# Performance work log

Measured on AMD Instinct MI355X. Metric: run time of the kernel, lower is better.

The kernel has to match this reference:

```python
import jax, jax.numpy as jnp
import numpy as np

C = 256
CK = C // 8  # query/key projection dim

def conv1x1(x, w, b):
    # x: (B,C,H,W), w: (O,C), b: (O,)
    return jnp.einsum('bchw,oc->bohw', x, w) + b[None, :, None, None]

def conv3x3(x, w, b):
    # w: (O,C,3,3)
    y = jax.lax.conv_general_dilated(x, w, window_strides=(1, 1), padding='SAME',
                                     dimension_numbers=('NCHW', 'OIHW', 'NCHW'))
    return y + b[None, :, None, None]

def setup_inputs() -> dict:
    key = jax.random.key(0)
    ks = jax.random.split(key, 24)
    s = 0.05
    d = {
        'x1': jax.random.normal(ks[0], (4, C, 64, 64), jnp.float32),
        'x2': jax.random.normal(ks[1], (4, C, 64, 64), jnp.float32),
        'wq1': jax.random.normal(ks[2], (CK, C), jnp.float32) * s,
        'bq1': jax.random.normal(ks[3], (CK,), jnp.float32) * s,
        'wk1': jax.random.normal(ks[4], (CK, C), jnp.float32) * s,
        'bk1': jax.random.normal(ks[5], (CK,), jnp.float32) * s,
        'wv1': jax.random.normal(ks[6], (C, C), jnp.float32) * s,
        'bv1': jax.random.normal(ks[7], (C,), jnp.float32) * s,
        'wq2': jax.random.normal(ks[8], (CK, C), jnp.float32) * s,
        'bq2': jax.random.normal(ks[9], (CK,), jnp.float32) * s,
        'wk2': jax.random.normal(ks[10], (CK, C), jnp.float32) * s,
        'bk2': jax.random.normal(ks[11], (CK,), jnp.float32) * s,
        'wv2': jax.random.normal(ks[12], (C, C), jnp.float32) * s,
        'bv2': jax.random.normal(ks[13], (C,), jnp.float32) * s,
        'wd1': jax.random.normal(ks[14], (C, C), jnp.float32) * s,
        'bd1': jax.random.normal(ks[15], (C,), jnp.float32) * s,
        'wd3': jax.random.normal(ks[16], (C, C, 3, 3), jnp.float32) * s,
        'bd3': jax.random.normal(ks[17], (C,), jnp.float32) * s,
        'gamma1': jax.random.normal(ks[18], (1,), jnp.float32) * 0.5,
        'gamma2': jax.random.normal(ks[19], (1,), jnp.float32) * 0.5,
    }
    return d

def reference(x1, x2, wq1, bq1, wk1, bk1, wv1, bv1, wq2, bq2, wk2, bk2, wv2, bv2,
              wd1, bd1, wd3, bd3, gamma1, gamma2):
    B, Cc, H, W = x1.shape
    N = H * W
    # projections (1x1 convs), flattened to (B, d, N)
    q1 = conv1x1(x1, wq1, bq1).reshape(B, CK, N)
    k1 = conv1x1(x1, wk1, bk1).reshape(B, CK, N)
    v1 = conv1x1(x1, wv1, bv1).reshape(B, Cc, N)
    q2 = conv1x1(x2, wq2, bq2).reshape(B, CK, N)
    k2 = conv1x1(x2, wk2, bk2).reshape(B, CK, N)
    v2 = conv1x1(x2, wv2, bv2).reshape(B, Cc, N)
    # cross attention 1: queries from x1, keys/values from x2
    energy1 = jnp.einsum('bdi,bdj->bij', q1, k2)          # (B,N,N)
    attn1 = jax.nn.softmax(energy1, axis=-1)
    out1 = jnp.einsum('bcj,bij->bci', v2, attn1).reshape(B, Cc, H, W)
    # cross attention 2: queries from x2, keys/values from x1
    energy2 = jnp.einsum('bdi,bdj->bij', q2, k1)
    attn2 = jax.nn.softmax(energy2, axis=-1)
    out2 = jnp.einsum('bcj,bij->bci', v1, attn2).reshape(B, Cc, H, W)
    # residual conv branches + gamma-scaled skip (norm1/norm2 in source are dead code)
    out1 = out1 + conv1x1(x1, wd1, bd1) + conv3x3(x1, wd3, bd3)
    out2 = out2 + conv1x1(x2, wd1, bd1) + conv3x3(x2, wd3, bd3)
    out1 = x1 + gamma1[0] * out1
    out2 = x2 + gamma2[0] * out2
    return (out1, out2)
```

## Files before the change

### kernel.cpp

```cpp
#include <hip/hip_runtime.h>
#include <hip/hip_bf16.h>

#define CC 256
#define CKD 32
#define NN 4096
#define HH 64
#define WW 64
#define BB 4

#define LOG2E 1.44269504088896f
#define EXPSHIFT 23.0831203874f

typedef __attribute__((ext_vector_type(8))) short short8;
typedef __attribute__((ext_vector_type(4))) float floatx4;

__device__ __forceinline__ unsigned f2bf(float f) {
  union { float f; unsigned u; } v; v.f = f;
  unsigned r = v.u + 0x7fffu + ((v.u >> 16) & 1u);
  return r >> 16;
}
__device__ __forceinline__ float fast_exp2(float x) {
#if __has_builtin(__builtin_amdgcn_exp2f)
  return __builtin_amdgcn_exp2f(x);
#else
  return __expf(x * 0.693147181f);
#endif
}
__device__ __forceinline__ float bf_lo(unsigned u) { return __uint_as_float(u << 16); }
__device__ __forceinline__ float bf_hi(unsigned u) { return __uint_as_float(u & 0xffff0000u); }

__device__ __forceinline__ void bar_lds() {
  asm volatile("s_waitcnt lgkmcnt(0)" ::: "memory");
  __builtin_amdgcn_s_barrier();
}

__global__ __launch_bounds__(256) void pack_kernel(
    const float* __restrict__ x1, const float* __restrict__ x2,
    unsigned short* __restrict__ Xp,
    const float* __restrict__ wd1, const float* __restrict__ wd3,
    const float* __restrict__ wq1, const float* __restrict__ wk1,
    const float* __restrict__ wv1,
    const float* __restrict__ wq2, const float* __restrict__ wk2,
    const float* __restrict__ wv2,
    const float* __restrict__ bq1, const float* __restrict__ bk1,
    const float* __restrict__ bv1,
    const float* __restrict__ bq2, const float* __restrict__ bk2,
    const float* __restrict__ bv2,
    unsigned short* __restrict__ Wp, unsigned short* __restrict__ Wqkv,
    float* __restrict__ Bias) {
  const int t = threadIdx.x;
  __shared__ float tile[64][65];
  if (blockIdx.z < 8) {
    const int nb = blockIdx.x, cbk = blockIdx.y, img = blockIdx.z;
    const float* X = ((img >> 2) ? x2 : x1) + (size_t)(img & 3) * CC * NN;
    const int n0 = nb * 64, c0 = cbk * 64;
    const int nl = t & 63, cl0 = t >> 6;
#pragma unroll
    for (int i = 0; i < 16; ++i)
      tile[cl0 + i * 4][nl] = X[(size_t)(c0 + cl0 + i * 4) * NN + n0 + nl];
    __syncthreads();
#pragma unroll
    for (int it = 0; it < 2; ++it) {
      int id = it * 256 + t;
      int nl2 = id >> 3, cc = id & 7;
      short8 v;
#pragma unroll
      for (int j = 0; j < 8; ++j) v[j] = (short)f2bf(tile[cc * 8 + j][nl2]);
      *(short8*)(Xp + (size_t)img * NN * CC + (size_t)(n0 + nl2) * CC + c0 + cc * 8) = v;
    }
  } else {
    const int id = (blockIdx.y * 64 + blockIdx.x) * 256 + t;
#pragma unroll
    for (int tap = 0; tap < 10; ++tap) {
      float v = (tap < 9) ? wd3[(size_t)id * 9 + tap] : wd1[id];
      Wp[(size_t)tap * (CC * CC) + id] = (unsigned short)f2bf(v);
    }
#pragma unroll
    for (int j = 0; j < 3; ++j) {
      int e = id + j * 65536;
      if (e < 2 * 320 * 256) {
        int inp = e / (320 * 256), rem = e % (320 * 256);
        int o = rem >> 8, c = rem & 255;
        float v;
        if (inp == 0)
          v = (o < 32) ? wq1[o * 256 + c] * LOG2E
              : (o < 64) ? wk1[(o - 32) * 256 + c] : wv1[(o - 64) * 256 + c];
        else
          v = (o < 32) ? wq2[o * 256 + c] * LOG2E
              : (o < 64) ? wk2[(o - 32) * 256 + c] : wv2[(o - 64) * 256 + c];
        Wqkv[e] = (unsigned short)f2bf(v);
      }
    }
    if (id < 640) {
      int inp = id / 320, o = id % 320;
      float v;
      if (inp == 0) v = (o < 32) ? bq1[o] * LOG2E
                        : (o < 64) ? bk1[o - 32] : bv1[o - 64];
      else          v = (o < 32) ? bq2[o] * LOG2E
                        : (o < 64) ? bk2[o - 32] : bv2[o - 64];
      Bias[id] = v;
    }
  }
}

__global__ __launch_bounds__(256) void proj_mfma_kernel(
    const unsigned short* __restrict__ Xp, const unsigned short* __restrict__ Wqkv,
    const float* __restrict__ Bias,
    unsigned short* __restrict__ Qp1, unsigned short* __restrict__ Kp1,
    unsigned short* __restrict__ Vp1,
    unsigned short* __restrict__ Qp2, unsigned short* __restrict__ Kp2,
    unsigned short* __restrict__ Vp2) {
  const int t = threadIdx.x;
  const int w = t >> 6, lane = t & 63;
  const int l15 = lane & 15, g = lane >> 4;
  const int img = blockIdx.x, pb = blockIdx.y;
  const int pix0 = pb * 64;
  const int inp = img >> 2, b = img & 3;
  const unsigned short* Xi = Xp + (size_t)img * NN * CC;
  const unsigned short* Wb = Wqkv + (size_t)inp * 320 * CC;
  const float* Bi = Bias + inp * 320;
  unsigned short* Qp = (inp ? Qp2 : Qp1) + (size_t)b * NN * CKD;
  unsigned short* Kp = (inp ? Kp2 : Kp1) + (size_t)b * NN * CKD;
  unsigned short* Vp = (inp ? Vp2 : Vp1) + (size_t)b * NN * CC;

  __shared__ unsigned short tile[320][72];

  floatx4 acc[4][5];
#pragma unroll
  for (int mf = 0; mf < 4; ++mf)
#pragma unroll
    for (int nf = 0; nf < 5; ++nf) acc[mf][nf] = (floatx4){0.f, 0.f, 0.f, 0.f};
  const int o0w = w * 80;

#pragma unroll
  for (int cb = 0; cb < 8; ++cb) {
    short8 a[4], bfr[5];
#pragma unroll
    for (int mf = 0; mf < 4; ++mf)
      a[mf] = *(const short8*)(Xi + (size_t)(pix0 + mf * 16 + l15) * CC + cb * 32 + g * 8);
#pragma unroll
    for (int nf = 0; nf < 5; ++nf)
      bfr[nf] = *(const short8*)(Wb + (size_t)(o0w + nf * 16 + l15) * CC + cb * 32 + g * 8);
#pragma unroll
    for (int nf = 0; nf < 5; ++nf)
#pragma unroll
      for (int mf = 0; mf < 4; ++mf)
        acc[mf][nf] = __builtin_amdgcn_mfma_f32_16x16x32_bf16(
            a[mf], bfr[nf], acc[mf][nf], 0, 0, 0);
  }

#pragma unroll
  for (int nf = 0; nf < 5; ++nf) {
    float bs = Bi[o0w + nf * 16 + l15];
#pragma unroll
    for (int mf = 0; mf < 4; ++mf) {
      uint2 pk;
      pk.x = f2bf(acc[mf][nf][0] + bs) | (f2bf(acc[mf][nf][1] + bs) << 16);
      pk.y = f2bf(acc[mf][nf][2] + bs) | (f2bf(acc[mf][nf][3] + bs) << 16);
      *(uint2*)&tile[o0w + nf * 16 + l15][mf * 16 + g * 4] = pk;
    }
  }
  __syncthreads();

  {
    const int pix = t >> 2, ch = t & 3;
    short8 vq, vk;
#pragma unroll
    for (int e = 0; e < 8; ++e) {
      vq[e] = (short)tile[ch * 8 + e][pix];
      vk[e] = (short)tile[32 + ch * 8 + e][pix];
    }
    *(short8*)(Qp + (size_t)(pix0 + pix) * CKD + ch * 8) = vq;
    *(short8*)(Kp + (size_t)(pix0 + pix) * CKD + ch * 8) = vk;
  }
#pragma unroll
  for (int it = 0; it < 8; ++it) {
    short8 vv = *(const short8*)&tile[64 + t][it * 8];
    *(short8*)(Vp + ((size_t)((pix0 >> 3) + it) * CC + t) * 8) = vv;
  }
}

__global__ __launch_bounds__(256, 2) void attn_kernel(
    const unsigned short* __restrict__ Qp1, const unsigned short* __restrict__ Kp1,
    const unsigned short* __restrict__ Qp2, const unsigned short* __restrict__ Kp2,
    const unsigned short* __restrict__ Vp1, const unsigned short* __restrict__ Vp2,
    const unsigned short* __restrict__ Xp, const unsigned short* __restrict__ Wp,
    const float* __restrict__ bd1, const float* __restrict__ bd3,
    const float* __restrict__ x1, const float* __restrict__ x2,
    const float* __restrict__ g1, const float* __restrict__ g2,
    float* __restrict__ out) {
  const int t = threadIdx.x;
  const int w = t >> 6, lane = t & 63;
  const int l15 = lane & 15, g = lane >> 4;
  const int att = blockIdx.x, b = blockIdx.y;
  const int yblk = blockIdx.z;
  const int i0 = yblk * 64;

  const unsigned short *Qp, *Kp, *Vp; const float *x; float gamma; float* o;
  if (att == 0) { Qp = Qp1; Kp = Kp2; Vp = Vp2; x = x1; gamma = g1[0]; o = out; }
  else          { Qp = Qp2; Kp = Kp1; Vp = Vp1; x = x2; gamma = g2[0];
                  o = out + (size_t)BB * CC * NN; }
  Qp += (size_t)b * NN * CKD; Kp += (size_t)b * NN * CKD; Vp += (size_t)b * NN * CC;
  x += (size_t)b * CC * NN; o += (size_t)b * CC * NN;
  const unsigned short* Xi = Xp + (size_t)(att * 4 + b) * NN * CC;

  __shared__ union {
    unsigned short ps[4][64][72];
    unsigned short xs[3][66][72];
  } u;
  __shared__ float l_s[64];

  short8 bq = *(const short8*)(Qp + (size_t)(i0 + w * 16 + l15) * CKD + g * 8);

  floatx4 acc[4][4];
#pragma unroll
  for (int a = 0; a < 4; ++a)
#pragma unroll
    for (int c = 0; c < 4; ++c) acc[a][c] = (floatx4){0.f, 0.f, 0.f, 0.f};
  float l_acc = 0.f;
  const floatx4 zinit = {-EXPSHIFT, -EXPSHIFT, -EXPSHIFT, -EXPSHIFT};

  short8 kr[2][4], vr[2][8];
  auto LOADK = [&](int tt, short8* d) {
    const unsigned short* kb = Kp + ((size_t)tt * 64 + l15) * CKD + g * 8;
#pragma unroll
    for (int js = 0; js < 4; ++js) d[js] = *(const short8*)(kb + js * 16 * CKD);
  };
  auto LOADV = [&](int tt, short8* d) {
#pragma unroll
    for (int ks = 0; ks < 2; ++ks)
#pragma unroll
      for (int cs = 0; cs < 4; ++cs)
        d[ks * 4 + cs] = *(const short8*)(Vp +
            (((size_t)tt * 8 + ks * 4 + g) * CC + (w * 64 + cs * 16 + l15)) * 8);
  };
  auto GEMM1 = [&](const short8* kb, unsigned short (*psb)[72]) {
#pragma unroll
    for (int js = 0; js < 4; ++js) {
      floatx4 s = __builtin_amdgcn_mfma_f32_16x16x32_bf16(kb[js], bq, zinit, 0, 0, 0);
      float p0 = fast_exp2(s[0]);
      float p1 = fast_exp2(s[1]);
      float p2 = fast_exp2(s[2]);
      float p3 = fast_exp2(s[3]);
      l_acc += (p0 + p1) + (p2 + p3);
      unsigned u0 = __float_as_uint(p0) + 0x8000u;
      unsigned u1 = __float_as_uint(p1) + 0x8000u;
      unsigned u2 = __float_as_uint(p2) + 0x8000u;
      unsigned u3 = __float_as_uint(p3) + 0x8000u;
      uint2 pk;
      pk.x = __builtin_amdgcn_perm(u1, u0, 0x07060302u);
      pk.y = __builtin_amdgcn_perm(u3, u2, 0x07060302u);
      *(uint2*)&psb[w * 16 + l15][js * 16 + g * 4] = pk;
    }
  };
  auto GEMM2 = [&](const short8* vb, unsigned short (*psb)[72]) {
#pragma unroll
    for (int ks = 0; ks < 2; ++ks) {
      short8 ap[4];
#pragma unroll
      for (int isub = 0; isub < 4; ++isub)
        ap[isub] = *(const short8*)&psb[isub * 16 + l15][ks * 32 + g * 8];
      __builtin_amdgcn_s_setprio(1);
#pragma unroll
      for (int cs = 0; cs < 4; ++cs)
#pragma unroll
        for (int isub = 0; isub < 4; ++isub)
          acc[isub][cs] = __builtin_amdgcn_mfma_f32_16x16x32_bf16(
              ap[isub], vb[ks * 4 + cs], acc[isub][cs], 0, 0, 0);
      __builtin_amdgcn_s_setprio(0);
    }
  };

  LOADK(0, kr[0]); LOADK(1, kr[1]);
  LOADV(0, vr[0]); LOADV(1, vr[1]);
  GEMM1(kr[0], u.ps[0]);
  GEMM1(kr[1], u.ps[1]);
  LOADK(2, kr[0]); LOADK(3, kr[1]);
  bar_lds();

  for (int jt = 0; jt < 64; jt += 2) {
    if (jt + 2 < 64) {
      GEMM1(kr[0], u.ps[(jt + 2) & 3]);
      if (jt + 4 < 64) LOADK(jt + 4, kr[0]);
    }
    GEMM2(vr[0], u.ps[jt & 3]);
    if (jt + 2 < 64) LOADV(jt + 2, vr[0]);
    if (jt + 3 < 64) {
      GEMM1(kr[1], u.ps[(jt + 3) & 3]);
      if (jt + 5 < 64) LOADK(jt + 5, kr[1]);
    }
    GEMM2(vr[1], u.ps[(jt + 1) & 3]);
    if (jt + 3 < 64) LOADV(jt + 3, vr[1]);
    if (jt + 2 < 64) bar_lds();
  }

  l_acc += __shfl_xor(l_acc, 16);
  l_acc += __shfl_xor(l_acc, 32);
  if (g == 0) l_s[w * 16 + l15] = l_acc;
  bar_lds();

#pragma unroll
  for (int isub = 0; isub < 4; ++isub) {
    float linv[4];
#pragma unroll
    for (int r = 0; r < 4; ++r) linv[r] = 1.f / l_s[isub * 16 + g * 4 + r];
#pragma unroll
    for (int cs = 0; cs < 4; ++cs)
#pragma unroll
      for (int r = 0; r < 4; ++r) acc[isub][cs][r] *= linv[r];
  }

  for (int cb = 0; cb < 4; ++cb) {
    const int c0 = cb * 64;
    if (cb) bar_lds();
#pragma unroll
    for (int it = 0; it < 7; ++it) {
      int id = it * 256 + t;
      if (id < 1584) {
        int r = id / 528, rem = id % 528;
        int col = rem >> 3, cc = rem & 7;
        int y = yblk - 1 + r, xx = col - 1;
        short8 v = {0, 0, 0, 0, 0, 0, 0, 0};
        if (y >= 0 && y < HH && xx >= 0 && xx < WW)
          v = *(const short8*)(Xi + (size_t)(y * WW + xx) * CC + c0 + cc * 8);
        *(short8*)&u.xs[r][col][cc * 8] = v;
      }
    }
    bar_lds();
#pragma unroll
    for (int tap = 0; tap < 10; ++tap) {
      const int dy = (tap < 9) ? tap / 3 - 1 : 0;
      const int dx = (tap < 9) ? tap % 3 - 1 : 0;
      const unsigned short* wrow =
          Wp + ((size_t)tap * CC + w * 64 + l15) * CC + c0 + g * 8;
#pragma unroll
      for (int ks = 0; ks < 2; ++ks) {
        short8 af[4], bw[4];
#pragma unroll
        for (int pm = 0; pm < 4; ++pm)
          af[pm] = *(const short8*)&u.xs[1 + dy][1 + pm * 16 + l15 + dx][ks * 32 + g * 8];
#pragma unroll
        for (int on = 0; on < 4; ++on)
          bw[on] = *(const short8*)(wrow + (size_t)(on * 16) * CC + ks * 32);
#pragma unroll
        for (int pm = 0; pm < 4; ++pm)
#pragma unroll
          for (int on = 0; on < 4; ++on)
            acc[pm][on] = __builtin_amdgcn_mfma_f32_16x16x32_bf16(
                af[pm], bw[on], acc[pm][on], 0, 0, 0);
      }
    }
  }

#pragma unroll
  for (int isub = 0; isub < 4; ++isub) {
#pragma unroll
    for (int cs = 0; cs < 4; ++cs) {
      int c = w * 64 + cs * 16 + l15;
      float bs = bd1[c] + bd3[c];
      size_t base = (size_t)c * NN + i0 + isub * 16 + g * 4;
      float4 xr = *(const float4*)(x + base);
      float4 ov;
      ov.x = xr.x + gamma * (acc[isub][cs][0] + bs);
      ov.y = xr.y + gamma * (acc[isub][cs][1] + bs);
      ov.z = xr.z + gamma * (acc[isub][cs][2] + bs);
      ov.w = xr.w + gamma * (acc[isub][cs][3] + bs);
      *(float4*)(o + base) = ov;
    }
  }
}

extern "C" void kernel_launch(void* const* d_in, const int* in_sizes, int n_in,
                              void* d_out, int out_size, void* d_ws, size_t ws_size,
                              hipStream_t stream) {
  const float* x1  = (const float*)d_in[0];
  const float* x2  = (const float*)d_in[1];
  const float* wq1 = (const float*)d_in[2];
  const float* bq1 = (const float*)d_in[3];
  const float* wk1 = (const float*)d_in[4];
  const float* bk1 = (const float*)d_in[5];
  const float* wv1 = (const float*)d_in[6];
  const float* bv1 = (const float*)d_in[7];
  const float* wq2 = (const float*)d_in[8];
  const float* bq2 = (const float*)d_in[9];
  const float* wk2 = (const float*)d_in[10];
  const float* bk2 = (const float*)d_in[11];
  const float* wv2 = (const float*)d_in[12];
  const float* bv2 = (const float*)d_in[13];
  const float* wd1 = (const float*)d_in[14];
  const float* bd1 = (const float*)d_in[15];
  const float* wd3 = (const float*)d_in[16];
  const float* bd3 = (const float*)d_in[17];
  const float* g1  = (const float*)d_in[18];
  const float* g2  = (const float*)d_in[19];
  float* out = (float*)d_out;

  const size_t QB = (size_t)BB * NN * CKD * 2;
  const size_t VB = (size_t)BB * NN * CC * 2;
  const size_t XB = (size_t)2 * BB * NN * CC * 2;
  const size_t WPB = (size_t)10 * CC * CC * 2;
  const size_t WQB = (size_t)2 * 320 * CC * 2;
  char* base = (char*)d_ws;
  unsigned short* Qp1 = (unsigned short*)(base);
  unsigned short* Kp1 = (unsigned short*)(base + QB);
  unsigned short* Qp2 = (unsigned short*)(base + 2 * QB);
  unsigned short* Kp2 = (unsigned short*)(base + 3 * QB);
  unsigned short* Vp1 = (unsigned short*)(base + 4 * QB);
  unsigned short* Vp2 = (unsigned short*)(base + 4 * QB + VB);
  unsigned short* Xp  = (unsigned short*)(base + 4 * QB + 2 * VB);
  unsigned short* Wp  = (unsigned short*)(base + 4 * QB + 2 * VB + XB);
  unsigned short* Wqkv = (unsigned short*)(base + 4 * QB + 2 * VB + XB + WPB);
  float* Bias = (float*)(base + 4 * QB + 2 * VB + XB + WPB + WQB);

  pack_kernel<<<dim3(NN / 64, CC / 64, 9), 256, 0, stream>>>(
      x1, x2, Xp, wd1, wd3, wq1, wk1, wv1, wq2, wk2, wv2,
      bq1, bk1, bv1, bq2, bk2, bv2, Wp, Wqkv, Bias);

  proj_mfma_kernel<<<dim3(2 * BB, NN / 64), 256, 0, stream>>>(
      Xp, Wqkv, Bias, Qp1, Kp1, Vp1, Qp2, Kp2, Vp2);

  attn_kernel<<<dim3(2, BB, NN / 64), 256, 0, stream>>>(
      Qp1, Kp1, Qp2, Kp2, Vp1, Vp2, Xp, Wp, bd1, bd3, x1, x2, g1, g2, out);
}
```

Before: 295.5 us.

## Keep softmax probabilities in registers, split attention into two channel-half passes

The attention kernel no longer writes the exponentiated scores to LDS. Each wave now owns 16 query rows, feeds its probabilities straight from the QK MFMA output into the PV MFMA as the A operand, and covers all 256 channels in two passes of 128. To make the register fragment match the MFMA layout, the V pack order in the pack kernel is permuted. This removes the per-tile LDS round trip and barriers, but the QK GEMM and exp now run twice, once per channel half, and the conv weight loads are spread across 16 output tiles per wave with less reuse.

```diff
diff --git a/kernel.cpp b/kernel.cpp
--- a/kernel.cpp
+++ b/kernel.cpp
@@ -26,8 +26,11 @@
   return __expf(x * 0.693147181f);
 #endif
 }
-__device__ __forceinline__ float bf_lo(unsigned u) { return __uint_as_float(u << 16); }
-__device__ __forceinline__ float bf_hi(unsigned u) { return __uint_as_float(u & 0xffff0000u); }
+__device__ __forceinline__ unsigned pack2bf(float a, float b) {
+  unsigned ua = __float_as_uint(a) + 0x8000u;
+  unsigned ub = __float_as_uint(b) + 0x8000u;
+  return __builtin_amdgcn_perm(ub, ua, 0x07060302u);
+}
 
 __device__ __forceinline__ void bar_lds() {
   asm volatile("s_waitcnt lgkmcnt(0)" ::: "memory");
@@ -174,9 +177,12 @@
     *(short8*)(Kp + (size_t)(pix0 + pix) * CKD + ch * 8) = vk;
   }
 #pragma unroll
-  for (int it = 0; it < 8; ++it) {
-    short8 vv = *(const short8*)&tile[64 + t][it * 8];
-    *(short8*)(Vp + ((size_t)((pix0 >> 3) + it) * CC + t) * 8) = vv;
+  for (int gi = 0; gi < 8; ++gi) {
+    const int h = gi >> 2, gg = gi & 3;
+    uint2 lo = *(const uint2*)&tile[64 + t][h * 32 + gg * 4];
+    uint2 hi = *(const uint2*)&tile[64 + t][h * 32 + 16 + gg * 4];
+    uint4 vv = {lo.x, lo.y, hi.x, hi.y};
+    *(uint4*)(Vp + (((size_t)(pix0 >> 3) + gi) * CC + t) * 8) = vv;
   }
 }
 
@@ -204,110 +210,105 @@
   x += (size_t)b * CC * NN; o += (size_t)b * CC * NN;
   const unsigned short* Xi = Xp + (size_t)(att * 4 + b) * NN * CC;
 
-  __shared__ union {
-    unsigned short ps[4][64][72];
-    unsigned short xs[3][66][72];
-  } u;
+  __shared__ unsigned short xs[3][66][72];
   __shared__ float l_s[64];
 
   short8 bq = *(const short8*)(Qp + (size_t)(i0 + w * 16 + l15) * CKD + g * 8);
 
-  floatx4 acc[4][4];
-#pragma unroll
-  for (int a = 0; a < 4; ++a)
-#pragma unroll
-    for (int c = 0; c < 4; ++c) acc[a][c] = (floatx4){0.f, 0.f, 0.f, 0.f};
+  floatx4 acc[16];
+#pragma unroll
+  for (int c16 = 0; c16 < 16; ++c16) acc[c16] = (floatx4){0.f, 0.f, 0.f, 0.f};
   float l_acc = 0.f;
   const floatx4 zinit = {-EXPSHIFT, -EXPSHIFT, -EXPSHIFT, -EXPSHIFT};
 
-  short8 kr[2][4], vr[2][8];
+  short8 kr0[4], kr1[4], vA[8], vB[8], paA[2], paB[2];
   auto LOADK = [&](int tt, short8* d) {
     const unsigned short* kb = Kp + ((size_t)tt * 64 + l15) * CKD + g * 8;
 #pragma unroll
     for (int js = 0; js < 4; ++js) d[js] = *(const short8*)(kb + js * 16 * CKD);
   };
-  auto LOADV = [&](int tt, short8* d) {
-#pragma unroll
-    for (int ks = 0; ks < 2; ++ks)
-#pragma unroll
-      for (int cs = 0; cs < 4; ++cs)
-        d[ks * 4 + cs] = *(const short8*)(Vp +
-            (((size_t)tt * 8 + ks * 4 + g) * CC + (w * 64 + cs * 16 + l15)) * 8);
+  auto LOADVH = [&](int tt, int h, int chalf, short8* d) {
+    const unsigned short* vb = Vp + (((size_t)tt * 8 + h * 4 + g) * CC + chalf + l15) * 8;
+#pragma unroll
+    for (int c8 = 0; c8 < 8; ++c8)
+      d[c8] = *(const short8*)(vb + (size_t)(c8 * 16) * 8);
   };
-  auto GEMM1 = [&](const short8* kb, unsigned short (*psb)[72]) {
-#pragma unroll
-    for (int js = 0; js < 4; ++js) {
-      floatx4 s = __builtin_amdgcn_mfma_f32_16x16x32_bf16(kb[js], bq, zinit, 0, 0, 0);
-      float p0 = fast_exp2(s[0]);
-      float p1 = fast_exp2(s[1]);
-      float p2 = fast_exp2(s[2]);
-      float p3 = fast_exp2(s[3]);
-      l_acc += (p0 + p1) + (p2 + p3);
-      unsigned u0 = __float_as_uint(p0) + 0x8000u;
-      unsigned u1 = __float_as_uint(p1) + 0x8000u;
-      unsigned u2 = __float_as_uint(p2) + 0x8000u;
-      unsigned u3 = __float_as_uint(p3) + 0x8000u;
-      uint2 pk;
-      pk.x = __builtin_amdgcn_perm(u1, u0, 0x07060302u);
-      pk.y = __builtin_amdgcn_perm(u3, u2, 0x07060302u);
-      *(uint2*)&psb[w * 16 + l15][js * 16 + g * 4] = pk;
-    }
+  auto G1 = [&](const short8* kb, short8* pa) {
+    floatx4 sA = __builtin_amdgcn_mfma_f32_16x16x32_bf16(kb[0], bq, zinit, 0, 0, 0);
+    floatx4 sB = __builtin_amdgcn_mfma_f32_16x16x32_bf16(kb[1], bq, zinit, 0, 0, 0);
+    floatx4 sC = __builtin_amdgcn_mfma_f32_16x16x32_bf16(kb[2], bq, zinit, 0, 0, 0);
+    floatx4 sD = __builtin_amdgcn_mfma_f32_16x16x32_bf16(kb[3], bq, zinit, 0, 0, 0);
+    float p0 = fast_exp2(sA[0]), p1 = fast_exp2(sA[1]);
+    float p2 = fast_exp2(sA[2]), p3 = fast_exp2(sA[3]);
+    float p4 = fast_exp2(sB[0]), p5 = fast_exp2(sB[1]);
+    float p6 = fast_exp2(sB[2]), p7 = fast_exp2(sB[3]);
+    float q0 = fast_exp2(sC[0]), q1 = fast_exp2(sC[1]);
+    float q2 = fast_exp2(sC[2]), q3 = fast_exp2(sC[3]);
+    float q4 = fast_exp2(sD[0]), q5 = fast_exp2(sD[1]);
+    float q6 = fast_exp2(sD[2]), q7 = fast_exp2(sD[3]);
+    l_acc += (((p0 + p1) + (p2 + p3)) + ((p4 + p5) + (p6 + p7)))
+           + (((q0 + q1) + (q2 + q3)) + ((q4 + q5) + (q6 + q7)));
+    union { unsigned u[4]; short8 s; } cv;
+    cv.u[0] = pack2bf(p0, p1); cv.u[1] = pack2bf(p2, p3);
+    cv.u[2] = pack2bf(p4, p5); cv.u[3] = pack2bf(p6, p7);
+    pa[0] = cv.s;
+    cv.u[0] = pack2bf(q0, q1); cv.u[1] = pack2bf(q2, q3);
+    cv.u[2] = pack2bf(q4, q5); cv.u[3] = pack2bf(q6, q7);
+    pa[1] = cv.s;
   };
-  auto GEMM2 = [&](const short8* vb, unsigned short (*psb)[72]) {
-#pragma unroll
-    for (int ks = 0; ks < 2; ++ks) {
-      short8 ap[4];
-#pragma unroll
-      for (int isub = 0; isub < 4; ++isub)
-        ap[isub] = *(const short8*)&psb[isub * 16 + l15][ks * 32 + g * 8];
+
+#pragma unroll
+  for (int p = 0; p < 2; ++p) {
+    const int chalf = p * 128;
+    const int ab = p * 8;
+    auto G2h = [&](const short8& pah, const short8* vb) {
       __builtin_amdgcn_s_setprio(1);
 #pragma unroll
-      for (int cs = 0; cs < 4; ++cs)
-#pragma unroll
-        for (int isub = 0; isub < 4; ++isub)
-          acc[isub][cs] = __builtin_amdgcn_mfma_f32_16x16x32_bf16(
-              ap[isub], vb[ks * 4 + cs], acc[isub][cs], 0, 0, 0);
+      for (int c8 = 0; c8 < 8; ++c8)
+        acc[ab + c8] = __builtin_amdgcn_mfma_f32_16x16x32_bf16(
+            pah, vb[c8], acc[ab + c8], 0, 0, 0);
       __builtin_amdgcn_s_setprio(0);
-    }
-  };
-
-  LOADK(0, kr[0]); LOADK(1, kr[1]);
-  LOADV(0, vr[0]); LOADV(1, vr[1]);
-  GEMM1(kr[0], u.ps[0]);
-  GEMM1(kr[1], u.ps[1]);
-  LOADK(2, kr[0]); LOADK(3, kr[1]);
-  bar_lds();
-
-  for (int jt = 0; jt < 64; jt += 2) {
-    if (jt + 2 < 64) {
-      GEMM1(kr[0], u.ps[(jt + 2) & 3]);
-      if (jt + 4 < 64) LOADK(jt + 4, kr[0]);
-    }
-    GEMM2(vr[0], u.ps[jt & 3]);
-    if (jt + 2 < 64) LOADV(jt + 2, vr[0]);
-    if (jt + 3 < 64) {
-      GEMM1(kr[1], u.ps[(jt + 3) & 3]);
-      if (jt + 5 < 64) LOADK(jt + 5, kr[1]);
-    }
-    GEMM2(vr[1], u.ps[(jt + 1) & 3]);
-    if (jt + 3 < 64) LOADV(jt + 3, vr[1]);
-    if (jt + 2 < 64) bar_lds();
-  }
-
-  l_acc += __shfl_xor(l_acc, 16);
-  l_acc += __shfl_xor(l_acc, 32);
-  if (g == 0) l_s[w * 16 + l15] = l_acc;
-  bar_lds();
-
-#pragma unroll
-  for (int isub = 0; isub < 4; ++isub) {
+    };
+
+    LOADK(0, kr0); LOADVH(0, 0, chalf, vA); LOADVH(0, 1, chalf, vB);
+    LOADK(1, kr1);
+    G1(kr0, paA);
+    LOADK(2, kr0);
+
+    for (int jt = 0; jt < 64; jt += 2) {
+      G1(kr1, paB);
+      if (jt + 3 < 64) LOADK(jt + 3, kr1);
+      G2h(paA[0], vA);
+      LOADVH(jt + 1, 0, chalf, vA);
+      G2h(paA[1], vB);
+      LOADVH(jt + 1, 1, chalf, vB);
+      if (jt + 2 < 64) {
+        G1(kr0, paA);
+        if (jt + 4 < 64) LOADK(jt + 4, kr0);
+      }
+      G2h(paB[0], vA);
+      if (jt + 2 < 64) LOADVH(jt + 2, 0, chalf, vA);
+      G2h(paB[1], vB);
+      if (jt + 2 < 64) LOADVH(jt + 2, 1, chalf, vB);
+    }
+
+    if (p == 0) {
+      float v = l_acc;
+      v += __shfl_xor(v, 16);
+      v += __shfl_xor(v, 32);
+      if (g == 0) l_s[w * 16 + l15] = v;
+      bar_lds();
+    }
+  }
+
+  {
     float linv[4];
 #pragma unroll
-    for (int r = 0; r < 4; ++r) linv[r] = 1.f / l_s[isub * 16 + g * 4 + r];
-#pragma unroll
-    for (int cs = 0; cs < 4; ++cs)
-#pragma unroll
-      for (int r = 0; r < 4; ++r) acc[isub][cs][r] *= linv[r];
+    for (int r = 0; r < 4; ++r) linv[r] = 1.f / l_s[w * 16 + g * 4 + r];
+#pragma unroll
+    for (int c16 = 0; c16 < 16; ++c16)
+#pragma unroll
+      for (int r = 0; r < 4; ++r) acc[c16][r] *= linv[r];
   }
 
   for (int cb = 0; cb < 4; ++cb) {
@@ -323,7 +324,7 @@
         short8 v = {0, 0, 0, 0, 0, 0, 0, 0};
         if (y >= 0 && y < HH && xx >= 0 && xx < WW)
           v = *(const short8*)(Xi + (size_t)(y * WW + xx) * CC + c0 + cc * 8);
-        *(short8*)&u.xs[r][col][cc * 8] = v;
+        *(short8*)&xs[r][col][cc * 8] = v;
       }
     }
     bar_lds();
@@ -331,42 +332,34 @@
     for (int tap = 0; tap < 10; ++tap) {
       const int dy = (tap < 9) ? tap / 3 - 1 : 0;
       const int dx = (tap < 9) ? tap % 3 - 1 : 0;
-      const unsigned short* wrow =
-          Wp + ((size_t)tap * CC + w * 64 + l15) * CC + c0 + g * 8;
 #pragma unroll
       for (int ks = 0; ks < 2; ++ks) {
-        short8 af[4], bw[4];
-#pragma unroll
-        for (int pm = 0; pm < 4; ++pm)
-          af[pm] = *(const short8*)&u.xs[1 + dy][1 + pm * 16 + l15 + dx][ks * 32 + g * 8];
-#pragma unroll
-        for (int on = 0; on < 4; ++on)
-          bw[on] = *(const short8*)(wrow + (size_t)(on * 16) * CC + ks * 32);
-#pragma unroll
-        for (int pm = 0; pm < 4; ++pm)
-#pragma unroll
-          for (int on = 0; on < 4; ++on)
-            acc[pm][on] = __builtin_amdgcn_mfma_f32_16x16x32_bf16(
-                af[pm], bw[on], acc[pm][on], 0, 0, 0);
+        short8 af = *(const short8*)
+            &xs[1 + dy][1 + w * 16 + l15 + dx][ks * 32 + g * 8];
+        const unsigned short* wrow =
+            Wp + ((size_t)tap * CC + l15) * CC + c0 + ks * 32 + g * 8;
+#pragma unroll
+        for (int c16 = 0; c16 < 16; ++c16) {
+          short8 bw = *(const short8*)(wrow + (size_t)(c16 * 16) * CC);
+          acc[c16] = __builtin_amdgcn_mfma_f32_16x16x32_bf16(
+              af, bw, acc[c16], 0, 0, 0);
+        }
       }
     }
   }
 
 #pragma unroll
-  for (int isub = 0; isub < 4; ++isub) {
-#pragma unroll
-    for (int cs = 0; cs < 4; ++cs) {
-      int c = w * 64 + cs * 16 + l15;
-      float bs = bd1[c] + bd3[c];
-      size_t base = (size_t)c * NN + i0 + isub * 16 + g * 4;
-      float4 xr = *(const float4*)(x + base);
-      float4 ov;
-      ov.x = xr.x + gamma * (acc[isub][cs][0] + bs);
-      ov.y = xr.y + gamma * (acc[isub][cs][1] + bs);
-      ov.z = xr.z + gamma * (acc[isub][cs][2] + bs);
-      ov.w = xr.w + gamma * (acc[isub][cs][3] + bs);
-      *(float4*)(o + base) = ov;
-    }
+  for (int c16 = 0; c16 < 16; ++c16) {
+    int c = c16 * 16 + l15;
+    float bs = bd1[c] + bd3[c];
+    size_t base = (size_t)c * NN + i0 + w * 16 + g * 4;
+    float4 xr = *(const float4*)(x + base);
+    float4 ov;
+    ov.x = xr.x + gamma * (acc[c16][0] + bs);
+    ov.y = xr.y + gamma * (acc[c16][1] + bs);
+    ov.z = xr.z + gamma * (acc[c16][2] + bs);
+    ov.w = xr.w + gamma * (acc[c16][3] + bs);
+    *(float4*)(o + base) = ov;
   }
 }
 
```

Result: slower. 623.5 us (+111.0%).

## Interleave conv-branch MFMAs into attention loop with separate accumulators

Applied to the files above, without the earlier changes.

Moves the 3x3+1x1 convolution work from a serial epilogue into the attention main loop. Halo tiles are loaded every eighth iteration and three conv k-steps are issued per other iteration into a separate accumulator set. V prefetch is split into half-tiles and K is single-buffered to offset the register cost. The aim is to overlap conv MFMAs with softmax exp and load latency. The cost is higher register pressure and more LDS, since the probability buffers no longer alias the halo tile.

```diff
diff --git a/kernel.cpp b/kernel.cpp
--- a/kernel.cpp
+++ b/kernel.cpp
@@ -26,8 +26,6 @@
   return __expf(x * 0.693147181f);
 #endif
 }
-__device__ __forceinline__ float bf_lo(unsigned u) { return __uint_as_float(u << 16); }
-__device__ __forceinline__ float bf_hi(unsigned u) { return __uint_as_float(u & 0xffff0000u); }
 
 __device__ __forceinline__ void bar_lds() {
   asm volatile("s_waitcnt lgkmcnt(0)" ::: "memory");
@@ -204,40 +202,42 @@
   x += (size_t)b * CC * NN; o += (size_t)b * CC * NN;
   const unsigned short* Xi = Xp + (size_t)(att * 4 + b) * NN * CC;
 
+  __shared__ unsigned short ps[4][64][72];
   __shared__ union {
-    unsigned short ps[4][64][72];
     unsigned short xs[3][66][72];
-  } u;
-  __shared__ float l_s[64];
+    float l_s[64];
+  } u2;
 
   short8 bq = *(const short8*)(Qp + (size_t)(i0 + w * 16 + l15) * CKD + g * 8);
 
   floatx4 acc[4][4];
+  floatx4 cac[4][4];
 #pragma unroll
   for (int a = 0; a < 4; ++a)
 #pragma unroll
-    for (int c = 0; c < 4; ++c) acc[a][c] = (floatx4){0.f, 0.f, 0.f, 0.f};
+    for (int c = 0; c < 4; ++c) {
+      acc[a][c] = (floatx4){0.f, 0.f, 0.f, 0.f};
+      cac[a][c] = (floatx4){0.f, 0.f, 0.f, 0.f};
+    }
   float l_acc = 0.f;
   const floatx4 zinit = {-EXPSHIFT, -EXPSHIFT, -EXPSHIFT, -EXPSHIFT};
 
-  short8 kr[2][4], vr[2][8];
-  auto LOADK = [&](int tt, short8* d) {
+  short8 kr[4], vA[4], vB[4];
+  auto LOADK = [&](int tt) {
     const unsigned short* kb = Kp + ((size_t)tt * 64 + l15) * CKD + g * 8;
 #pragma unroll
-    for (int js = 0; js < 4; ++js) d[js] = *(const short8*)(kb + js * 16 * CKD);
+    for (int js = 0; js < 4; ++js) kr[js] = *(const short8*)(kb + js * 16 * CKD);
   };
-  auto LOADV = [&](int tt, short8* d) {
-#pragma unroll
-    for (int ks = 0; ks < 2; ++ks)
-#pragma unroll
-      for (int cs = 0; cs < 4; ++cs)
-        d[ks * 4 + cs] = *(const short8*)(Vp +
-            (((size_t)tt * 8 + ks * 4 + g) * CC + (w * 64 + cs * 16 + l15)) * 8);
+  auto LOADVH = [&](int tt, int ks, short8* d) {
+#pragma unroll
+    for (int cs = 0; cs < 4; ++cs)
+      d[cs] = *(const short8*)(Vp +
+          (((size_t)tt * 8 + ks * 4 + g) * CC + (w * 64 + cs * 16 + l15)) * 8);
   };
-  auto GEMM1 = [&](const short8* kb, unsigned short (*psb)[72]) {
+  auto GEMM1 = [&](unsigned short (*psb)[72]) {
 #pragma unroll
     for (int js = 0; js < 4; ++js) {
-      floatx4 s = __builtin_amdgcn_mfma_f32_16x16x32_bf16(kb[js], bq, zinit, 0, 0, 0);
+      floatx4 s = __builtin_amdgcn_mfma_f32_16x16x32_bf16(kr[js], bq, zinit, 0, 0, 0);
       float p0 = fast_exp2(s[0]);
       float p1 = fast_exp2(s[1]);
       float p2 = fast_exp2(s[2]);
@@ -245,115 +245,108 @@
       l_acc += (p0 + p1) + (p2 + p3);
       unsigned u0 = __float_as_uint(p0) + 0x8000u;
       unsigned u1 = __float_as_uint(p1) + 0x8000u;
-      unsigned u2 = __float_as_uint(p2) + 0x8000u;
+      unsigned u2v = __float_as_uint(p2) + 0x8000u;
       unsigned u3 = __float_as_uint(p3) + 0x8000u;
       uint2 pk;
       pk.x = __builtin_amdgcn_perm(u1, u0, 0x07060302u);
-      pk.y = __builtin_amdgcn_perm(u3, u2, 0x07060302u);
+      pk.y = __builtin_amdgcn_perm(u3, u2v, 0x07060302u);
       *(uint2*)&psb[w * 16 + l15][js * 16 + g * 4] = pk;
     }
   };
-  auto GEMM2 = [&](const short8* vb, unsigned short (*psb)[72]) {
-#pragma unroll
-    for (int ks = 0; ks < 2; ++ks) {
-      short8 ap[4];
+  auto G2ks = [&](int ks, const short8* vb, unsigned short (*psb)[72]) {
+    short8 ap[4];
+#pragma unroll
+    for (int isub = 0; isub < 4; ++isub)
+      ap[isub] = *(const short8*)&psb[isub * 16 + l15][ks * 32 + g * 8];
+    __builtin_amdgcn_s_setprio(1);
+#pragma unroll
+    for (int cs = 0; cs < 4; ++cs)
 #pragma unroll
       for (int isub = 0; isub < 4; ++isub)
-        ap[isub] = *(const short8*)&psb[isub * 16 + l15][ks * 32 + g * 8];
-      __builtin_amdgcn_s_setprio(1);
-#pragma unroll
-      for (int cs = 0; cs < 4; ++cs)
-#pragma unroll
-        for (int isub = 0; isub < 4; ++isub)
-          acc[isub][cs] = __builtin_amdgcn_mfma_f32_16x16x32_bf16(
-              ap[isub], vb[ks * 4 + cs], acc[isub][cs], 0, 0, 0);
-      __builtin_amdgcn_s_setprio(0);
-    }
+        acc[isub][cs] = __builtin_amdgcn_mfma_f32_16x16x32_bf16(
+            ap[isub], vb[cs], acc[isub][cs], 0, 0, 0);
+    __builtin_amdgcn_s_setprio(0);
   };
 
-  LOADK(0, kr[0]); LOADK(1, kr[1]);
-  LOADV(0, vr[0]); LOADV(1, vr[1]);
-  GEMM1(kr[0], u.ps[0]);
-  GEMM1(kr[1], u.ps[1]);
-  LOADK(2, kr[0]); LOADK(3, kr[1]);
+  LOADK(0); LOADVH(0, 0, vA); LOADVH(0, 1, vB);
+  GEMM1(ps[0]);
+  LOADK(1);
+  GEMM1(ps[1]);
+  LOADK(2);
   bar_lds();
 
   for (int jt = 0; jt < 64; jt += 2) {
+    const int r = jt >> 1;
+    const int cb = r >> 3, rc = r & 7;
+    const int c0 = cb * 64;
+
+    if (rc == 0) {
+#pragma unroll
+      for (int it = 0; it < 7; ++it) {
+        int id = it * 256 + t;
+        if (id < 1584) {
+          int rr = id / 528, rem = id % 528;
+          int col = rem >> 3, ccc = rem & 7;
+          int y = yblk - 1 + rr, xx = col - 1;
+          short8 v = {0, 0, 0, 0, 0, 0, 0, 0};
+          if (y >= 0 && y < HH && xx >= 0 && xx < WW)
+            v = *(const short8*)(Xi + (size_t)(y * WW + xx) * CC + c0 + ccc * 8);
+          *(short8*)&u2.xs[rr][col][ccc * 8] = v;
+        }
+      }
+    } else {
+#pragma unroll
+      for (int k = 0; k < 3; ++k) {
+        const int uu = (rc - 1) * 3 + k;
+        if (uu < 20) {
+          const int tap = uu >> 1, ks2 = uu & 1;
+          const int dy = (tap < 9) ? tap / 3 - 1 : 0;
+          const int dx = (tap < 9) ? tap % 3 - 1 : 0;
+          const unsigned short* wrow =
+              Wp + ((size_t)tap * CC + w * 64 + l15) * CC + c0 + g * 8;
+          short8 af[4], bw[4];
+#pragma unroll
+          for (int pm = 0; pm < 4; ++pm)
+            af[pm] = *(const short8*)
+                &u2.xs[1 + dy][1 + pm * 16 + l15 + dx][ks2 * 32 + g * 8];
+#pragma unroll
+          for (int on = 0; on < 4; ++on)
+            bw[on] = *(const short8*)(wrow + (size_t)(on * 16) * CC + ks2 * 32);
+#pragma unroll
+          for (int pm = 0; pm < 4; ++pm)
+#pragma unroll
+            for (int on = 0; on < 4; ++on)
+              cac[pm][on] = __builtin_amdgcn_mfma_f32_16x16x32_bf16(
+                  af[pm], bw[on], cac[pm][on], 0, 0, 0);
+        }
+      }
+    }
+
     if (jt + 2 < 64) {
-      GEMM1(kr[0], u.ps[(jt + 2) & 3]);
-      if (jt + 4 < 64) LOADK(jt + 4, kr[0]);
-    }
-    GEMM2(vr[0], u.ps[jt & 3]);
-    if (jt + 2 < 64) LOADV(jt + 2, vr[0]);
+      GEMM1(ps[(jt + 2) & 3]);
+      if (jt + 3 < 64) LOADK(jt + 3);
+    }
+    G2ks(0, vA, ps[jt & 3]);   LOADVH(jt + 1, 0, vA);
+    G2ks(1, vB, ps[jt & 3]);   LOADVH(jt + 1, 1, vB);
     if (jt + 3 < 64) {
-      GEMM1(kr[1], u.ps[(jt + 3) & 3]);
-      if (jt + 5 < 64) LOADK(jt + 5, kr[1]);
-    }
-    GEMM2(vr[1], u.ps[(jt + 1) & 3]);
-    if (jt + 3 < 64) LOADV(jt + 3, vr[1]);
-    if (jt + 2 < 64) bar_lds();
+      GEMM1(ps[(jt + 3) & 3]);
+      if (jt + 4 < 64) LOADK(jt + 4);
+    }
+    G2ks(0, vA, ps[(jt + 1) & 3]); if (jt + 2 < 64) LOADVH(jt + 2, 0, vA);
+    G2ks(1, vB, ps[(jt + 1) & 3]); if (jt + 2 < 64) LOADVH(jt + 2, 1, vB);
+    bar_lds();
   }
 
   l_acc += __shfl_xor(l_acc, 16);
   l_acc += __shfl_xor(l_acc, 32);
-  if (g == 0) l_s[w * 16 + l15] = l_acc;
+  if (g == 0) u2.l_s[w * 16 + l15] = l_acc;
   bar_lds();
 
 #pragma unroll
   for (int isub = 0; isub < 4; ++isub) {
     float linv[4];
 #pragma unroll
-    for (int r = 0; r < 4; ++r) linv[r] = 1.f / l_s[isub * 16 + g * 4 + r];
-#pragma unroll
-    for (int cs = 0; cs < 4; ++cs)
-#pragma unroll
-      for (int r = 0; r < 4; ++r) acc[isub][cs][r] *= linv[r];
-  }
-
-  for (int cb = 0; cb < 4; ++cb) {
-    const int c0 = cb * 64;
-    if (cb) bar_lds();
-#pragma unroll
-    for (int it = 0; it < 7; ++it) {
-      int id = it * 256 + t;
-      if (id < 1584) {
-        int r = id / 528, rem = id % 528;
-        int col = rem >> 3, cc = rem & 7;
-        int y = yblk - 1 + r, xx = col - 1;
-        short8 v = {0, 0, 0, 0, 0, 0, 0, 0};
-        if (y >= 0 && y < HH && xx >= 0 && xx < WW)
-          v = *(const short8*)(Xi + (size_t)(y * WW + xx) * CC + c0 + cc * 8);
-        *(short8*)&u.xs[r][col][cc * 8] = v;
-      }
-    }
-    bar_lds();
-#pragma unroll
-    for (int tap = 0; tap < 10; ++tap) {
-      const int dy = (tap < 9) ? tap / 3 - 1 : 0;
-      const int dx = (tap < 9) ? tap % 3 - 1 : 0;
-      const unsigned short* wrow =
-          Wp + ((size_t)tap * CC + w * 64 + l15) * CC + c0 + g * 8;
-#pragma unroll
-      for (int ks = 0; ks < 2; ++ks) {
-        short8 af[4], bw[4];
-#pragma unroll
-        for (int pm = 0; pm < 4; ++pm)
-          af[pm] = *(const short8*)&u.xs[1 + dy][1 + pm * 16 + l15 + dx][ks * 32 + g * 8];
-#pragma unroll
-        for (int on = 0; on < 4; ++on)
-          bw[on] = *(const short8*)(wrow + (size_t)(on * 16) * CC + ks * 32);
-#pragma unroll
-        for (int pm = 0; pm < 4; ++pm)
-#pragma unroll
-          for (int on = 0; on < 4; ++on)
-            acc[pm][on] = __builtin_amdgcn_mfma_f32_16x16x32_bf16(
-                af[pm], bw[on], acc[pm][on], 0, 0, 0);
-      }
-    }
-  }
-
-#pragma unroll
-  for (int isub = 0; isub < 4; ++isub) {
+    for (int r2 = 0; r2 < 4; ++r2) linv[r2] = 1.f / u2.l_s[isub * 16 + g * 4 + r2];
 #pragma unroll
     for (int cs = 0; cs < 4; ++cs) {
       int c = w * 64 + cs * 16 + l15;
@@ -361,10 +354,10 @@
       size_t base = (size_t)c * NN + i0 + isub * 16 + g * 4;
       float4 xr = *(const float4*)(x + base);
       float4 ov;
-      ov.x = xr.x + gamma * (acc[isub][cs][0] + bs);
-      ov.y = xr.y + gamma * (acc[isub][cs][1] + bs);
-      ov.z = xr.z + gamma * (acc[isub][cs][2] + bs);
-      ov.w = xr.w + gamma * (acc[isub][cs][3] + bs);
+      ov.x = xr.x + gamma * (acc[isub][cs][0] * linv[0] + cac[isub][cs][0] + bs);
+      ov.y = xr.y + gamma * (acc[isub][cs][1] * linv[1] + cac[isub][cs][1] + bs);
+      ov.z = xr.z + gamma * (acc[isub][cs][2] * linv[2] + cac[isub][cs][2] + bs);
+      ov.w = xr.w + gamma * (acc[isub][cs][3] * linv[3] + cac[isub][cs][3] + bs);
       *(float4*)(o + base) = ov;
     }
   }
```

New measurement: 506.3 us. 71.3% more time.
